# Performance work log

Measured on AMD Instinct MI355X. Metric: run time of the kernel, lower is better.

Reference implementation:

```python
import jax, jax.numpy as jnp
import numpy as np

D, H, DFF, K, S = 512, 8, 2048, 4, 4
DH = D // H
SHAPES = [(56, 56), (28, 28), (14, 14), (7, 7)]
B = 4


def setup_inputs() -> dict:
    key = jax.random.key(0)
    ks = jax.random.split(key, 32)
    inp = {}
    for i, (hl, wl) in enumerate(SHAPES):
        inp[f'src{i}'] = jax.random.normal(ks[i], (B, hl, wl, D), jnp.float32)
        inp[f'ref{i}'] = jax.random.uniform(ks[4 + i], (B, hl, wl, 2), jnp.float32)
    def lin(k, fan_in, fan_out):
        return jax.random.normal(k, (fan_in, fan_out), jnp.float32) * (1.0 / np.sqrt(fan_in))
    inp['Wv'] = lin(ks[8], D, D)
    inp['bv'] = jnp.zeros((D,), jnp.float32)
    inp['Woff'] = jax.random.normal(ks[9], (D, H * S * K * 2), jnp.float32) * 0.01
    inp['boff'] = jax.random.normal(ks[10], (H * S * K * 2,), jnp.float32) * 0.1
    inp['Wattn'] = jax.random.normal(ks[11], (D, H * S * K), jnp.float32) * 0.01
    inp['battn'] = jnp.zeros((H * S * K,), jnp.float32)
    inp['Wo'] = lin(ks[12], D, D)
    inp['bo'] = jnp.zeros((D,), jnp.float32)
    inp['W1'] = lin(ks[13], D, DFF)
    inp['b1'] = jnp.zeros((DFF,), jnp.float32)
    inp['W2'] = lin(ks[14], DFF, D)
    inp['b2'] = jnp.zeros((D,), jnp.float32)
    inp['g1'] = jnp.ones((D,), jnp.float32)
    inp['be1'] = jnp.zeros((D,), jnp.float32)
    inp['g2'] = jnp.ones((D,), jnp.float32)
    inp['be2'] = jnp.zeros((D,), jnp.float32)
    return inp


def layernorm(x, g, b, eps=1e-5):
    mu = jnp.mean(x, axis=-1, keepdims=True)
    var = jnp.mean(jnp.square(x - mu), axis=-1, keepdims=True)
    return (x - mu) * jax.lax.rsqrt(var + eps) * g + b


def bilinear_sample(value, loc):
    # value: [B, Hl, Wl, H, DH] per-scale projected values; loc: [B, Lq, H, K, 2] in [0,1]
    b, hl, wl, h, dh = value.shape
    x = loc[..., 0] * wl - 0.5
    y = loc[..., 1] * hl - 0.5
    x0f = jnp.floor(x); y0f = jnp.floor(y)
    wx1 = x - x0f; wx0 = 1.0 - wx1
    wy1 = y - y0f; wy0 = 1.0 - wy1
    x0 = x0f.astype(jnp.int32); y0 = y0f.astype(jnp.int32)
    vflat = value.transpose(0, 3, 1, 2, 4).reshape(b, h, hl * wl, dh)  # [B,H,HW,DH]

    def corner(xi, yi, w):
        valid = ((xi >= 0) & (xi < wl) & (yi >= 0) & (yi < hl)).astype(value.dtype)
        idx = jnp.clip(yi, 0, hl - 1) * wl + jnp.clip(xi, 0, wl - 1)  # [B,Lq,H,K]
        idx = idx.transpose(0, 2, 1, 3)  # [B,H,Lq,K]
        lq, kk = idx.shape[2], idx.shape[3]
        g = jnp.take_along_axis(vflat, idx.reshape(b, h, lq * kk)[..., None], axis=2)
        g = g.reshape(b, h, lq, kk, dh)
        wv = (w * valid).transpose(0, 2, 1, 3)[..., None]  # [B,H,Lq,K,1]
        return g * wv

    out = (corner(x0, y0, wx0 * wy0) + corner(x0 + 1, y0, wx1 * wy0)
           + corner(x0, y0 + 1, wx0 * wy1) + corner(x0 + 1, y0 + 1, wx1 * wy1))
    return out.transpose(0, 2, 1, 3, 4)  # [B,Lq,H,K,DH]


def _forward(src0, src1, src2, src3, ref0, ref1, ref2, ref3,
             Wv, bv, Woff, boff, Wattn, battn, Wo, bo, W1, b1, W2, b2, g1, be1, g2, be2):
    srcs = [src0, src1, src2, src3]
    refs = [ref0, ref1, ref2, ref3]
    # shared value projection per scale, split into heads
    values = [(s @ Wv + bv).reshape(s.shape[0], s.shape[1], s.shape[2], H, DH) for s in srcs]
    outs = []
    for src_l, ref_l in zip(srcs, refs):
        b = src_l.shape[0]
        q = src_l.reshape(b, -1, D)          # [B,Lq,D]
        ref = ref_l.reshape(b, -1, 2)        # [B,Lq,2]
        lq = q.shape[1]
        off = (q @ Woff + boff).reshape(b, lq, H, S, K, 2)
        attn = jax.nn.softmax((q @ Wattn + battn).reshape(b, lq, H, S * K), axis=-1)
        attn = attn.reshape(b, lq, H, S, K)
        acc = jnp.zeros((b, lq, H, DH), q.dtype)
        for li, (v, (hl, wl)) in enumerate(zip(values, SHAPES)):
            scale = jnp.array([wl, hl], q.dtype)
            loc = ref[:, :, None, None, :] + off[:, :, :, li] / scale  # [B,Lq,H,K,2]
            samp = bilinear_sample(v, loc)                              # [B,Lq,H,K,DH]
            acc = acc + jnp.einsum('blhk,blhkd->blhd', attn[:, :, :, li], samp)
        a = acc.reshape(b, lq, D) @ Wo + bo
        x = layernorm(q + a, g1, be1)
        f = jax.nn.relu(x @ W1 + b1) @ W2 + b2
        x = layernorm(x + f, g2, be2)
        outs.append(x)
    return jnp.concatenate(outs, axis=1)  # [B, sum(Hl*Wl), D]


def reference(src0, src1, src2, src3, ref0, ref1, ref2, ref3,
              Wv, bv, Woff, boff, Wattn, battn, Wo, bo, W1, b1, W2, b2, g1, be1, g2, be2):
    return _forward(src0, src1, src2, src3, ref0, ref1, ref2, ref3,
                    Wv, bv, Woff, boff, Wattn, battn, Wo, bo, W1, b1, W2, b2, g1, be1, g2, be2)
```

## Files before the change

kernel.cpp:

```cpp
#include <hip/hip_runtime.h>
#include <math.h>


#define TTOT 16660
#define TPAD 16768
#define LQTOT 4165

typedef __attribute__((ext_vector_type(8))) short bf16x8;
typedef __attribute__((ext_vector_type(4))) float f32x4;

typedef __attribute__((address_space(1))) const unsigned int g_u32;
typedef __attribute__((address_space(3))) unsigned int l_u32;

__device__ __forceinline__ unsigned short f2bf(float f) {
    unsigned u = __builtin_bit_cast(unsigned, f);
    u += 0x7fffu + ((u >> 16) & 1u);
    return (unsigned short)(u >> 16);
}
__device__ __forceinline__ float bf2f(unsigned short s) {
    unsigned u = ((unsigned)s) << 16;
    return __builtin_bit_cast(float, u);
}
__device__ __forceinline__ float bflo(unsigned u) {
    return __builtin_bit_cast(float, u << 16);
}
__device__ __forceinline__ float bfhi(unsigned u) {
    return __builtin_bit_cast(float, u & 0xffff0000u);
}

__device__ __forceinline__ int permute_row(int t) {
    int off, area, qoff;
    if (t < 12544)      { off = 0;     area = 3136; qoff = 0;    }
    else if (t < 15680) { off = 12544; area = 784;  qoff = 3136; }
    else if (t < 16464) { off = 15680; area = 196;  qoff = 3920; }
    else                { off = 16464; area = 49;   qoff = 4116; }
    int rel = t - off;
    int b = rel / area;
    int pos = rel - b * area;
    return b * LQTOT + qoff + pos;
}

__device__ __forceinline__ const float* src_row(int row, const float* s0, const float* s1,
                                                const float* s2, const float* s3) {
    if (row < 12544) return s0 + (size_t)row * 512;
    if (row < 15680) return s1 + (size_t)(row - 12544) * 512;
    if (row < 16464) return s2 + (size_t)(row - 15680) * 512;
    return s3 + (size_t)(row - 16464) * 512;
}

__device__ __forceinline__ void async_copy16(const unsigned short* g, unsigned short* lds_wave_uniform) {
    __builtin_amdgcn_global_load_lds((g_u32*)g, (l_u32*)lds_wave_uniform, 16, 0, 0);
}

enum { EPI_SPLIT = 0, EPI_RESID_SRC = 1, EPI_RELU = 2, EPI_RESID_SCATTER = 3 };

struct GemmArgs {
    const unsigned short* A;
    const unsigned short* Bt;
    const float* bias0; const float* bias1; const float* bias2;
    const unsigned short* residb;
    const float* s0; const float* s1; const float* s2; const float* s3;
    void* out0; unsigned short* out1; unsigned short* out2;
    int M, N, Kd;
};

template <int EPI>
__global__ __launch_bounds__(256) void gemm_mfma(GemmArgs a)
{
    __shared__ unsigned short As[128 * 32];
    __shared__ unsigned short Bs[128 * 32];
    const int tid  = threadIdx.x;
    const int wave = tid >> 6;
    const int lane = tid & 63;
    const int m0 = blockIdx.y * 128;
    const int n0 = blockIdx.x * 128;

    const int srow = tid >> 2;
    const int kg   = (tid & 3) ^ ((tid >> 3) & 3);
    const unsigned short* Ag = a.A  + (size_t)(m0 + srow) * a.Kd + kg * 8;
    const unsigned short* Bg = a.Bt + (size_t)(n0 + srow) * a.Kd + kg * 8;
    const size_t rstep = (size_t)64 * a.Kd;
    unsigned short* ldsA0 = As + wave * 512;
    unsigned short* ldsA1 = As + 2048 + wave * 512;
    unsigned short* ldsB0 = Bs + wave * 512;
    unsigned short* ldsB1 = Bs + 2048 + wave * 512;

    const int wm = (wave >> 1) << 6;
    const int wn = (wave & 1) << 6;
    const int fm = lane & 15;
    const int fq = lane >> 4;
    const int slot = (fq ^ ((fm >> 1) & 3)) << 3;

    const f32x4 fzero = {0.f, 0.f, 0.f, 0.f};
    f32x4 acc[4][4];
#pragma unroll
    for (int i = 0; i < 4; ++i)
#pragma unroll
        for (int j = 0; j < 4; ++j) acc[i][j] = fzero;

    for (int k0 = 0; k0 < a.Kd; k0 += 32) {
        __syncthreads();
        async_copy16(Ag + k0,         ldsA0);
        async_copy16(Ag + rstep + k0, ldsA1);
        async_copy16(Bg + k0,         ldsB0);
        async_copy16(Bg + rstep + k0, ldsB1);
        __syncthreads();
        bf16x8 af[4], bfr[4];
#pragma unroll
        for (int mt = 0; mt < 4; ++mt)
            af[mt] = *(const bf16x8*)&As[(wm + mt * 16 + fm) * 32 + slot];
#pragma unroll
        for (int nt = 0; nt < 4; ++nt)
            bfr[nt] = *(const bf16x8*)&Bs[(wn + nt * 16 + fm) * 32 + slot];
#pragma unroll
        for (int mt = 0; mt < 4; ++mt)
#pragma unroll
            for (int nt = 0; nt < 4; ++nt)
                acc[mt][nt] = __builtin_amdgcn_mfma_f32_16x16x32_bf16(
                    af[mt], bfr[nt], acc[mt][nt], 0, 0, 0);
    }

    const int cn0 = n0 + wn + fm;
    int cols[4]; float bi[4];
#pragma unroll
    for (int nt = 0; nt < 4; ++nt) {
        const int c = cn0 + nt * 16;
        cols[nt] = c;
        if (EPI == EPI_SPLIT)
            bi[nt] = (c < 512) ? a.bias0[c] : (c < 768) ? a.bias1[c - 512] : a.bias2[c - 768];
        else
            bi[nt] = a.bias0[c];
    }
#pragma unroll
    for (int mt = 0; mt < 4; ++mt) {
#pragma unroll
        for (int r = 0; r < 4; ++r) {
            const int row = m0 + wm + mt * 16 + fq * 4 + r;
            if (row >= a.M) continue;
            const size_t ro = (size_t)row;
            const float* srcres = (EPI == EPI_RESID_SRC)
                                  ? src_row(row, a.s0, a.s1, a.s2, a.s3) : nullptr;
#pragma unroll
            for (int nt = 0; nt < 4; ++nt) {
                float v = acc[mt][nt][r] + bi[nt];
                const int c = cols[nt];
                if (EPI == EPI_SPLIT) {
                    if (c < 512)      ((unsigned short*)a.out0)[ro * 512 + c]        = f2bf(v);
                    else if (c < 768) a.out1[ro * 256 + (c - 512)]                   = f2bf(v);
                    else              a.out2[ro * 128 + (c - 768)]                   = f2bf(v);
                } else if (EPI == EPI_RESID_SRC) {
                    v += srcres[c];
                    ((unsigned short*)a.out0)[ro * 512 + c] = f2bf(v);
                } else if (EPI == EPI_RELU) {
                    v = fmaxf(v, 0.f);
                    ((unsigned short*)a.out0)[ro * 2048 + c] = f2bf(v);
                } else {
                    v += bf2f(a.residb[ro * 512 + c]);
                    ((float*)a.out0)[(size_t)permute_row(row) * 512 + c] = v;
                }
            }
        }
    }
}

struct PrepArgs {
    const float *Wv, *Woff, *Wattn, *Wo, *W1, *W2;
    unsigned short *Wcat, *Wot, *W1t, *W2t;
    const float *s0, *s1, *s2, *s3;
    unsigned short* Qb;
};

__global__ __launch_bounds__(256) void prep(PrepArgs p)
{
    __shared__ unsigned short t[32][33];
    const int bid = blockIdx.x;
    if (bid < 2752) {
        const float* W; unsigned short* Wt; int K, N, lbx, rel;
        if (bid < 256)       { W = p.Wv;    Wt = p.Wcat;                   K = 512;  N = 512;  lbx = 4; rel = bid; }
        else if (bid < 384)  { W = p.Woff;  Wt = p.Wcat + (size_t)512*512; K = 512;  N = 256;  lbx = 3; rel = bid - 256; }
        else if (bid < 448)  { W = p.Wattn; Wt = p.Wcat + (size_t)768*512; K = 512;  N = 128;  lbx = 2; rel = bid - 384; }
        else if (bid < 704)  { W = p.Wo;    Wt = p.Wot;                    K = 512;  N = 512;  lbx = 4; rel = bid - 448; }
        else if (bid < 1728) { W = p.W1;    Wt = p.W1t;                    K = 512;  N = 2048; lbx = 6; rel = bid - 704; }
        else                 { W = p.W2;    Wt = p.W2t;                    K = 2048; N = 512;  lbx = 4; rel = bid - 1728; }
        const int bx = rel & ((1 << lbx) - 1);
        const int by = rel >> lbx;
        const int tx = threadIdx.x & 31, ty = threadIdx.x >> 5;
        const int nb = bx * 32, kb = by * 32;
#pragma unroll
        for (int j = 0; j < 32; j += 8)
            t[ty + j][tx] = f2bf(W[(size_t)(kb + ty + j) * N + nb + tx]);
        __syncthreads();
#pragma unroll
        for (int j = 0; j < 32; j += 8)
            Wt[(size_t)(nb + ty + j) * K + kb + tx] = t[tx][ty + j];
    } else {
        const int gid = (bid - 2752) * 256 + threadIdx.x;
        const int e = gid * 4;
        const int row = e >> 9, col = e & 511;
        const float* sr = src_row(row, p.s0, p.s1, p.s2, p.s3);
        const float4 v = *(const float4*)(sr + col);
        ushort4 o;
        o.x = f2bf(v.x); o.y = f2bf(v.y); o.z = f2bf(v.z); o.w = f2bf(v.w);
        *(ushort4*)(p.Qb + (size_t)row * 512 + col) = o;
    }
}

__global__ __launch_bounds__(256) void sample_attn(
    const unsigned short* __restrict__ Vp, const unsigned short* __restrict__ OFFB,
    const unsigned short* __restrict__ ATT,
    const float* __restrict__ rf0, const float* __restrict__ rf1,
    const float* __restrict__ rf2, const float* __restrict__ rf3,
    unsigned short* __restrict__ ACCb)
{
    __shared__ int   midx[4][2][16][4];
    __shared__ float mw[4][2][16][4];
    const int wave = threadIdx.x >> 6;
    const int lane = threadIdx.x & 63;
    const int t  = blockIdx.x;
    const int hp = wave;

    int soff, area;
    const float* rp;
    if (t < 12544)      { soff = 0;     area = 3136; rp = rf0 + (size_t)t * 2; }
    else if (t < 15680) { soff = 12544; area = 784;  rp = rf1 + (size_t)(t - 12544) * 2; }
    else if (t < 16464) { soff = 15680; area = 196;  rp = rf2 + (size_t)(t - 15680) * 2; }
    else                { soff = 16464; area = 49;   rp = rf3 + (size_t)(t - 16464) * 2; }
    const int b = (t - soff) / area;

    if (lane < 32) {
        const int hl = lane >> 4;
        const int s  = lane & 15;
        const int h  = hp * 2 + hl;
        const int li = s >> 2;
        float logit = bf2f(ATT[(size_t)t * 128 + h * 16 + s]);
        float mx = logit;
#pragma unroll
        for (int o = 8; o > 0; o >>= 1) mx = fmaxf(mx, __shfl_xor(mx, o, 16));
        float e = __expf(logit - mx);
        float sumv = e;
#pragma unroll
        for (int o = 8; o > 0; o >>= 1) sumv += __shfl_xor(sumv, o, 16);
        const float ew = e / sumv;

        const int wl = 56 >> li;
        const int lvlbase = (li == 0) ? 0 : (li == 1) ? 12544 : (li == 2) ? 15680 : 16464;
        const int base = lvlbase + b * wl * wl;
        const float rx = rp[0], ry = rp[1];
        const unsigned off2 = *(const unsigned*)(OFFB + (size_t)t * 256 + h * 32 + s * 2);
        const float ox = bflo(off2);
        const float oy = bfhi(off2);
        const float x = rx * (float)wl + ox - 0.5f;
        const float y = ry * (float)wl + oy - 0.5f;
        const float x0f = floorf(x), y0f = floorf(y);
        const float wx1 = x - x0f, wx0 = 1.f - wx1;
        const float wy1 = y - y0f, wy0 = 1.f - wy1;
        const int x0 = (int)x0f, y0 = (int)y0f;
        const int x1 = x0 + 1, y1 = y0 + 1;
        const int xc0 = min(max(x0, 0), wl - 1), xc1 = min(max(x1, 0), wl - 1);
        const int yc0 = min(max(y0, 0), wl - 1), yc1 = min(max(y1, 0), wl - 1);
        const float fx0 = (x0 >= 0 && x0 < wl) ? 1.f : 0.f;
        const float fx1 = (x1 >= 0 && x1 < wl) ? 1.f : 0.f;
        const float fy0 = (y0 >= 0 && y0 < wl) ? 1.f : 0.f;
        const float fy1 = (y1 >= 0 && y1 < wl) ? 1.f : 0.f;
        const int hb2 = h * 128;
        midx[wave][hl][s][0] = (base + yc0 * wl + xc0) * 1024 + hb2;
        midx[wave][hl][s][1] = (base + yc0 * wl + xc1) * 1024 + hb2;
        midx[wave][hl][s][2] = (base + yc1 * wl + xc0) * 1024 + hb2;
        midx[wave][hl][s][3] = (base + yc1 * wl + xc1) * 1024 + hb2;
        mw[wave][hl][s][0] = wx0 * wy0 * fx0 * fy0 * ew;
        mw[wave][hl][s][1] = wx1 * wy0 * fx1 * fy0 * ew;
        mw[wave][hl][s][2] = wx0 * wy1 * fx0 * fy1 * ew;
        mw[wave][hl][s][3] = wx1 * wy1 * fx1 * fy1 * ew;
    }
    __syncthreads();

    const int hl = lane >> 5;
    const int laneoff = (lane & 31) * 4;
    const char* vb = (const char*)Vp;
    float accL = 0.f, accH = 0.f;
#pragma unroll
    for (int s = 0; s < 16; ++s) {
        const int4   I = *(const int4*)&midx[wave][hl][s][0];
        const float4 W = *(const float4*)&mw[wave][hl][s][0];
        const unsigned u0 = *(const unsigned*)(vb + (I.x + laneoff));
        const unsigned u1 = *(const unsigned*)(vb + (I.y + laneoff));
        const unsigned u2 = *(const unsigned*)(vb + (I.z + laneoff));
        const unsigned u3 = *(const unsigned*)(vb + (I.w + laneoff));
        accL += W.x * bflo(u0); accH += W.x * bfhi(u0);
        accL += W.y * bflo(u1); accH += W.y * bfhi(u1);
        accL += W.z * bflo(u2); accH += W.z * bfhi(u2);
        accL += W.w * bflo(u3); accH += W.w * bfhi(u3);
    }
    const int h = hp * 2 + hl;
    ushort2 o;
    o.x = f2bf(accL);
    o.y = f2bf(accH);
    *(ushort2*)((char*)ACCb + (size_t)t * 1024 + h * 128 + laneoff) = o;
}

__global__ __launch_bounds__(256) void ln_bf16(
    unsigned short* __restrict__ X, const float* __restrict__ g, const float* __restrict__ be)
{
    const int row = blockIdx.x;
    unsigned short* xr = X + (size_t)row * 512;
    const int tid = threadIdx.x;
    float v0 = bf2f(xr[tid]);
    float v1 = bf2f(xr[tid + 256]);
    float s = v0 + v1;
    float ss = v0 * v0 + v1 * v1;
#pragma unroll
    for (int o = 32; o > 0; o >>= 1) {
        s += __shfl_down(s, o, 64);
        ss += __shfl_down(ss, o, 64);
    }
    __shared__ float sm[4], sm2[4];
    const int w = tid >> 6;
    if ((tid & 63) == 0) { sm[w] = s; sm2[w] = ss; }
    __syncthreads();
    if (tid == 0) {
        sm[0] = sm[0] + sm[1] + sm[2] + sm[3];
        sm2[0] = sm2[0] + sm2[1] + sm2[2] + sm2[3];
    }
    __syncthreads();
    const float mu = sm[0] * (1.f / 512.f);
    const float var = sm2[0] * (1.f / 512.f) - mu * mu;
    const float rs = rsqrtf(var + 1e-5f);
    xr[tid]       = f2bf((v0 - mu) * rs * g[tid]       + be[tid]);
    xr[tid + 256] = f2bf((v1 - mu) * rs * g[tid + 256] + be[tid + 256]);
}

__global__ __launch_bounds__(256) void ln_f32(
    float* __restrict__ X, const float* __restrict__ g, const float* __restrict__ be)
{
    const int row = blockIdx.x;
    float* xr = X + (size_t)row * 512;
    const int tid = threadIdx.x;
    float v0 = xr[tid];
    float v1 = xr[tid + 256];
    float s = v0 + v1;
    float ss = v0 * v0 + v1 * v1;
#pragma unroll
    for (int o = 32; o > 0; o >>= 1) {
        s += __shfl_down(s, o, 64);
        ss += __shfl_down(ss, o, 64);
    }
    __shared__ float sm[4], sm2[4];
    const int w = tid >> 6;
    if ((tid & 63) == 0) { sm[w] = s; sm2[w] = ss; }
    __syncthreads();
    if (tid == 0) {
        sm[0] = sm[0] + sm[1] + sm[2] + sm[3];
        sm2[0] = sm2[0] + sm2[1] + sm2[2] + sm2[3];
    }
    __syncthreads();
    const float mu = sm[0] * (1.f / 512.f);
    const float var = sm2[0] * (1.f / 512.f) - mu * mu;
    const float rs = rsqrtf(var + 1e-5f);
    xr[tid]       = (v0 - mu) * rs * g[tid]       + be[tid];
    xr[tid + 256] = (v1 - mu) * rs * g[tid + 256] + be[tid + 256];
}

extern "C" void kernel_launch(void* const* d_in, const int* in_sizes, int n_in,
                              void* d_out, int out_size, void* d_ws, size_t ws_size,
                              hipStream_t stream)
{
    const float* src[4] = { (const float*)d_in[0], (const float*)d_in[2],
                            (const float*)d_in[4], (const float*)d_in[6] };
    const float* ref[4] = { (const float*)d_in[1], (const float*)d_in[3],
                            (const float*)d_in[5], (const float*)d_in[7] };
    const float* Wv    = (const float*)d_in[8];
    const float* bv    = (const float*)d_in[9];
    const float* Woff  = (const float*)d_in[10];
    const float* boff  = (const float*)d_in[11];
    const float* Wattn = (const float*)d_in[12];
    const float* battn = (const float*)d_in[13];
    const float* Wo    = (const float*)d_in[14];
    const float* bo    = (const float*)d_in[15];
    const float* W1    = (const float*)d_in[16];
    const float* b1    = (const float*)d_in[17];
    const float* W2    = (const float*)d_in[18];
    const float* b2    = (const float*)d_in[19];
    const float* g1    = (const float*)d_in[20];
    const float* be1   = (const float*)d_in[21];
    const float* g2    = (const float*)d_in[22];
    const float* be2   = (const float*)d_in[23];

    unsigned short* w    = (unsigned short*)d_ws;
    unsigned short* Qb   = w;
    unsigned short* Vp   = Qb   + (size_t)TPAD * 512;
    unsigned short* OFFB = Vp   + (size_t)TPAD * 512;
    unsigned short* ATT  = OFFB + (size_t)TPAD * 256;
    unsigned short* ACCb = ATT  + (size_t)TPAD * 128;
    unsigned short* X1b  = ACCb + (size_t)TPAD * 512;
    unsigned short* Fb   = X1b  + (size_t)TPAD * 512;
    unsigned short* Wcat = Fb   + (size_t)TPAD * 2048;
    unsigned short* Wot  = Wcat + (size_t)896 * 512;
    unsigned short* W1t  = Wot  + (size_t)512 * 512;
    unsigned short* W2t  = W1t  + (size_t)2048 * 512;

    const dim3 blk(256);

    PrepArgs pp = {};
    pp.Wv = Wv; pp.Woff = Woff; pp.Wattn = Wattn; pp.Wo = Wo; pp.W1 = W1; pp.W2 = W2;
    pp.Wcat = Wcat; pp.Wot = Wot; pp.W1t = W1t; pp.W2t = W2t;
    pp.s0 = src[0]; pp.s1 = src[1]; pp.s2 = src[2]; pp.s3 = src[3];
    pp.Qb = Qb;
    prep<<<dim3(11082), blk, 0, stream>>>(pp);

    GemmArgs a1 = {};
    a1.A = Qb; a1.Bt = Wcat; a1.bias0 = bv; a1.bias1 = boff; a1.bias2 = battn;
    a1.out0 = Vp; a1.out1 = OFFB; a1.out2 = ATT; a1.M = TTOT; a1.N = 896; a1.Kd = 512;
    gemm_mfma<EPI_SPLIT><<<dim3(7, 131), blk, 0, stream>>>(a1);

    sample_attn<<<dim3(TTOT), blk, 0, stream>>>(Vp, OFFB, ATT,
                                                ref[0], ref[1], ref[2], ref[3], ACCb);

    GemmArgs a2 = {};
    a2.A = ACCb; a2.Bt = Wot; a2.bias0 = bo;
    a2.s0 = src[0]; a2.s1 = src[1]; a2.s2 = src[2]; a2.s3 = src[3];
    a2.out0 = X1b; a2.M = TTOT; a2.N = 512; a2.Kd = 512;
    gemm_mfma<EPI_RESID_SRC><<<dim3(4, 131), blk, 0, stream>>>(a2);

    ln_bf16<<<dim3(TTOT), blk, 0, stream>>>(X1b, g1, be1);

    GemmArgs a3 = {};
    a3.A = X1b; a3.Bt = W1t; a3.bias0 = b1;
    a3.out0 = Fb; a3.M = TTOT; a3.N = 2048; a3.Kd = 512;
    gemm_mfma<EPI_RELU><<<dim3(16, 131), blk, 0, stream>>>(a3);

    GemmArgs a4 = {};
    a4.A = Fb; a4.Bt = W2t; a4.bias0 = b2; a4.residb = X1b;
    a4.out0 = d_out; a4.M = TTOT; a4.N = 512; a4.Kd = 2048;
    gemm_mfma<EPI_RESID_SCATTER><<<dim3(4, 131), blk, 0, stream>>>(a4);

    ln_f32<<<dim3(TTOT), blk, 0, stream>>>((float*)d_out, g2, be2);
}
```

Baseline: 423.9 us.

## Add 64-row GEMM tiles for N=512 GEMMs and widen sampling per thread

Templates the MFMA GEMM on the M tile size and launches the two N=512 GEMMs (output projection and FFN down-projection) with 64-row tiles, doubling their block count so more CUs have work. Separately, the deformable sampling kernel now handles two tokens per block: all 256 threads compute the sampling metadata, and each lane gathers 8 bytes (4 bf16 channels) per corner instead of 4. The aim is better occupancy on the small-N GEMMs and fewer, wider gathers with less idle work in the sampler. The cost is lower data reuse per tile in the 64-row GEMMs.

```diff
diff --git a/kernel.cpp b/kernel.cpp
--- a/kernel.cpp
+++ b/kernel.cpp
@@ -64,15 +64,16 @@
     int M, N, Kd;
 };
 
-template <int EPI>
+template <int EPI, int TM>
 __global__ __launch_bounds__(256) void gemm_mfma(GemmArgs a)
 {
-    __shared__ unsigned short As[128 * 32];
+    constexpr int MT = TM / 32;
+    __shared__ unsigned short As[TM * 32];
     __shared__ unsigned short Bs[128 * 32];
     const int tid  = threadIdx.x;
     const int wave = tid >> 6;
     const int lane = tid & 63;
-    const int m0 = blockIdx.y * 128;
+    const int m0 = blockIdx.y * TM;
     const int n0 = blockIdx.x * 128;
 
     const int srow = tid >> 2;
@@ -85,35 +86,35 @@
     unsigned short* ldsB0 = Bs + wave * 512;
     unsigned short* ldsB1 = Bs + 2048 + wave * 512;
 
-    const int wm = (wave >> 1) << 6;
+    const int wm = (wave >> 1) * (MT * 16);
     const int wn = (wave & 1) << 6;
     const int fm = lane & 15;
     const int fq = lane >> 4;
     const int slot = (fq ^ ((fm >> 1) & 3)) << 3;
 
     const f32x4 fzero = {0.f, 0.f, 0.f, 0.f};
-    f32x4 acc[4][4];
-#pragma unroll
-    for (int i = 0; i < 4; ++i)
+    f32x4 acc[MT][4];
+#pragma unroll
+    for (int i = 0; i < MT; ++i)
 #pragma unroll
         for (int j = 0; j < 4; ++j) acc[i][j] = fzero;
 
     for (int k0 = 0; k0 < a.Kd; k0 += 32) {
         __syncthreads();
-        async_copy16(Ag + k0,         ldsA0);
-        async_copy16(Ag + rstep + k0, ldsA1);
+        async_copy16(Ag + k0, ldsA0);
+        if (TM == 128) async_copy16(Ag + rstep + k0, ldsA1);
         async_copy16(Bg + k0,         ldsB0);
         async_copy16(Bg + rstep + k0, ldsB1);
         __syncthreads();
-        bf16x8 af[4], bfr[4];
-#pragma unroll
-        for (int mt = 0; mt < 4; ++mt)
+        bf16x8 af[MT], bfr[4];
+#pragma unroll
+        for (int mt = 0; mt < MT; ++mt)
             af[mt] = *(const bf16x8*)&As[(wm + mt * 16 + fm) * 32 + slot];
 #pragma unroll
         for (int nt = 0; nt < 4; ++nt)
             bfr[nt] = *(const bf16x8*)&Bs[(wn + nt * 16 + fm) * 32 + slot];
 #pragma unroll
-        for (int mt = 0; mt < 4; ++mt)
+        for (int mt = 0; mt < MT; ++mt)
 #pragma unroll
             for (int nt = 0; nt < 4; ++nt)
                 acc[mt][nt] = __builtin_amdgcn_mfma_f32_16x16x32_bf16(
@@ -132,7 +133,7 @@
             bi[nt] = a.bias0[c];
     }
 #pragma unroll
-    for (int mt = 0; mt < 4; ++mt) {
+    for (int mt = 0; mt < MT; ++mt) {
 #pragma unroll
         for (int r = 0; r < 4; ++r) {
             const int row = m0 + wm + mt * 16 + fq * 4 + r;
@@ -212,26 +213,25 @@
     const float* __restrict__ rf2, const float* __restrict__ rf3,
     unsigned short* __restrict__ ACCb)
 {
-    __shared__ int   midx[4][2][16][4];
-    __shared__ float mw[4][2][16][4];
-    const int wave = threadIdx.x >> 6;
-    const int lane = threadIdx.x & 63;
-    const int t  = blockIdx.x;
-    const int hp = wave;
-
-    int soff, area;
-    const float* rp;
-    if (t < 12544)      { soff = 0;     area = 3136; rp = rf0 + (size_t)t * 2; }
-    else if (t < 15680) { soff = 12544; area = 784;  rp = rf1 + (size_t)(t - 12544) * 2; }
-    else if (t < 16464) { soff = 15680; area = 196;  rp = rf2 + (size_t)(t - 15680) * 2; }
-    else                { soff = 16464; area = 49;   rp = rf3 + (size_t)(t - 16464) * 2; }
-    const int b = (t - soff) / area;
-
-    if (lane < 32) {
-        const int hl = lane >> 4;
-        const int s  = lane & 15;
-        const int h  = hp * 2 + hl;
+    __shared__ int   midx[2][8][16][4];
+    __shared__ float mw[2][8][16][4];
+    const int tid = threadIdx.x;
+
+    {
+        const int tl = tid >> 7;
+        const int h  = (tid >> 4) & 7;
+        const int s  = tid & 15;
+        const int t  = blockIdx.x * 2 + tl;
         const int li = s >> 2;
+
+        int soff, area;
+        const float* rp;
+        if (t < 12544)      { soff = 0;     area = 3136; rp = rf0 + (size_t)t * 2; }
+        else if (t < 15680) { soff = 12544; area = 784;  rp = rf1 + (size_t)(t - 12544) * 2; }
+        else if (t < 16464) { soff = 15680; area = 196;  rp = rf2 + (size_t)(t - 15680) * 2; }
+        else                { soff = 16464; area = 49;   rp = rf3 + (size_t)(t - 16464) * 2; }
+        const int b = (t - soff) / area;
+
         float logit = bf2f(ATT[(size_t)t * 128 + h * 16 + s]);
         float mx = logit;
 #pragma unroll
@@ -263,39 +263,41 @@
         const float fy0 = (y0 >= 0 && y0 < wl) ? 1.f : 0.f;
         const float fy1 = (y1 >= 0 && y1 < wl) ? 1.f : 0.f;
         const int hb2 = h * 128;
-        midx[wave][hl][s][0] = (base + yc0 * wl + xc0) * 1024 + hb2;
-        midx[wave][hl][s][1] = (base + yc0 * wl + xc1) * 1024 + hb2;
-        midx[wave][hl][s][2] = (base + yc1 * wl + xc0) * 1024 + hb2;
-        midx[wave][hl][s][3] = (base + yc1 * wl + xc1) * 1024 + hb2;
-        mw[wave][hl][s][0] = wx0 * wy0 * fx0 * fy0 * ew;
-        mw[wave][hl][s][1] = wx1 * wy0 * fx1 * fy0 * ew;
-        mw[wave][hl][s][2] = wx0 * wy1 * fx0 * fy1 * ew;
-        mw[wave][hl][s][3] = wx1 * wy1 * fx1 * fy1 * ew;
+        midx[tl][h][s][0] = (base + yc0 * wl + xc0) * 1024 + hb2;
+        midx[tl][h][s][1] = (base + yc0 * wl + xc1) * 1024 + hb2;
+        midx[tl][h][s][2] = (base + yc1 * wl + xc0) * 1024 + hb2;
+        midx[tl][h][s][3] = (base + yc1 * wl + xc1) * 1024 + hb2;
+        mw[tl][h][s][0] = wx0 * wy0 * fx0 * fy0 * ew;
+        mw[tl][h][s][1] = wx1 * wy0 * fx1 * fy0 * ew;
+        mw[tl][h][s][2] = wx0 * wy1 * fx0 * fy1 * ew;
+        mw[tl][h][s][3] = wx1 * wy1 * fx1 * fy1 * ew;
     }
     __syncthreads();
 
-    const int hl = lane >> 5;
-    const int laneoff = (lane & 31) * 4;
+    const int wave = tid >> 6;
+    const int lane = tid & 63;
+    const int tl = wave >> 1;
+    const int h  = (wave & 1) * 4 + (lane >> 4);
+    const int t  = blockIdx.x * 2 + tl;
+    const int off8 = (lane & 15) * 8;
     const char* vb = (const char*)Vp;
-    float accL = 0.f, accH = 0.f;
+    float a0 = 0.f, a1 = 0.f, a2 = 0.f, a3 = 0.f;
 #pragma unroll
     for (int s = 0; s < 16; ++s) {
-        const int4   I = *(const int4*)&midx[wave][hl][s][0];
-        const float4 W = *(const float4*)&mw[wave][hl][s][0];
-        const unsigned u0 = *(const unsigned*)(vb + (I.x + laneoff));
-        const unsigned u1 = *(const unsigned*)(vb + (I.y + laneoff));
-        const unsigned u2 = *(const unsigned*)(vb + (I.z + laneoff));
-        const unsigned u3 = *(const unsigned*)(vb + (I.w + laneoff));
-        accL += W.x * bflo(u0); accH += W.x * bfhi(u0);
-        accL += W.y * bflo(u1); accH += W.y * bfhi(u1);
-        accL += W.z * bflo(u2); accH += W.z * bfhi(u2);
-        accL += W.w * bflo(u3); accH += W.w * bfhi(u3);
-    }
-    const int h = hp * 2 + hl;
-    ushort2 o;
-    o.x = f2bf(accL);
-    o.y = f2bf(accH);
-    *(ushort2*)((char*)ACCb + (size_t)t * 1024 + h * 128 + laneoff) = o;
+        const int4   I = *(const int4*)&midx[tl][h][s][0];
+        const float4 W = *(const float4*)&mw[tl][h][s][0];
+        const uint2 u0 = *(const uint2*)(vb + (I.x + off8));
+        const uint2 u1 = *(const uint2*)(vb + (I.y + off8));
+        const uint2 u2 = *(const uint2*)(vb + (I.z + off8));
+        const uint2 u3 = *(const uint2*)(vb + (I.w + off8));
+        a0 += W.x * bflo(u0.x); a1 += W.x * bfhi(u0.x); a2 += W.x * bflo(u0.y); a3 += W.x * bfhi(u0.y);
+        a0 += W.y * bflo(u1.x); a1 += W.y * bfhi(u1.x); a2 += W.y * bflo(u1.y); a3 += W.y * bfhi(u1.y);
+        a0 += W.z * bflo(u2.x); a1 += W.z * bfhi(u2.x); a2 += W.z * bflo(u2.y); a3 += W.z * bfhi(u2.y);
+        a0 += W.w * bflo(u3.x); a1 += W.w * bfhi(u3.x); a2 += W.w * bflo(u3.y); a3 += W.w * bfhi(u3.y);
+    }
+    ushort4 o;
+    o.x = f2bf(a0); o.y = f2bf(a1); o.z = f2bf(a2); o.w = f2bf(a3);
+    *(ushort4*)((char*)ACCb + (size_t)t * 1024 + h * 128 + off8) = o;
 }
 
 __global__ __launch_bounds__(256) void ln_bf16(
@@ -410,28 +412,28 @@
     GemmArgs a1 = {};
     a1.A = Qb; a1.Bt = Wcat; a1.bias0 = bv; a1.bias1 = boff; a1.bias2 = battn;
     a1.out0 = Vp; a1.out1 = OFFB; a1.out2 = ATT; a1.M = TTOT; a1.N = 896; a1.Kd = 512;
-    gemm_mfma<EPI_SPLIT><<<dim3(7, 131), blk, 0, stream>>>(a1);
-
-    sample_attn<<<dim3(TTOT), blk, 0, stream>>>(Vp, OFFB, ATT,
-                                                ref[0], ref[1], ref[2], ref[3], ACCb);
+    gemm_mfma<EPI_SPLIT, 128><<<dim3(7, 131), blk, 0, stream>>>(a1);
+
+    sample_attn<<<dim3(TTOT / 2), blk, 0, stream>>>(Vp, OFFB, ATT,
+                                                    ref[0], ref[1], ref[2], ref[3], ACCb);
 
     GemmArgs a2 = {};
     a2.A = ACCb; a2.Bt = Wot; a2.bias0 = bo;
     a2.s0 = src[0]; a2.s1 = src[1]; a2.s2 = src[2]; a2.s3 = src[3];
     a2.out0 = X1b; a2.M = TTOT; a2.N = 512; a2.Kd = 512;
-    gemm_mfma<EPI_RESID_SRC><<<dim3(4, 131), blk, 0, stream>>>(a2);
+    gemm_mfma<EPI_RESID_SRC, 64><<<dim3(4, 262), blk, 0, stream>>>(a2);
 
     ln_bf16<<<dim3(TTOT), blk, 0, stream>>>(X1b, g1, be1);
 
     GemmArgs a3 = {};
     a3.A = X1b; a3.Bt = W1t; a3.bias0 = b1;
     a3.out0 = Fb; a3.M = TTOT; a3.N = 2048; a3.Kd = 512;
-    gemm_mfma<EPI_RELU><<<dim3(16, 131), blk, 0, stream>>>(a3);
+    gemm_mfma<EPI_RELU, 128><<<dim3(16, 131), blk, 0, stream>>>(a3);
 
     GemmArgs a4 = {};
     a4.A = Fb; a4.Bt = W2t; a4.bias0 = b2; a4.residb = X1b;
     a4.out0 = d_out; a4.M = TTOT; a4.N = 512; a4.Kd = 2048;
-    gemm_mfma<EPI_RESID_SCATTER><<<dim3(4, 131), blk, 0, stream>>>(a4);
+    gemm_mfma<EPI_RESID_SCATTER, 64><<<dim3(4, 262), blk, 0, stream>>>(a4);
 
     ln_f32<<<dim3(TTOT), blk, 0, stream>>>((float*)d_out, g2, be2);
 }
```

Measured after the change: 440.7 us. 1.04x slower.
